# Kernel optimization log

Hardware: AMD Instinct MI355X
Metric: run time of the kernel (lower is better)

## Reference

```python
import jax, jax.numpy as jnp
import numpy as np

B, T, H, OUT = 65536, 24, 64, 2  # batch, window, num_neurons, 2*predicted_step
P_LAYER, P_TIME = 0.2, 0.2


def _mask(k, p):
    # bernoulli(1-p)/(1-p) variational dropout mask on [B, H]
    return jax.random.bernoulli(k, 1.0 - p, (B, H)).astype(jnp.float32) / (1.0 - p)


def setup_inputs() -> dict:
    key = jax.random.key(0)
    ks = jax.random.split(key, 20)
    u = 1.0 / np.sqrt(H)  # torch LSTMCell default init: U(-1/sqrt(H), 1/sqrt(H))
    xav = np.sqrt(2.0 / (B + H))  # xavier_normal_ std for [B, H] states
    inp = {
        "x": jax.random.normal(ks[0], (B, T, 1), dtype=jnp.float32),
        # LSTMCell 1: input dim 1 -> H; gates stacked [i, f, g, o] like torch
        "W_ih1": jax.random.uniform(ks[1], (4 * H, 1), minval=-u, maxval=u),
        "W_hh1": jax.random.uniform(ks[2], (4 * H, H), minval=-u, maxval=u),
        "b_ih1": jax.random.uniform(ks[3], (4 * H,), minval=-u, maxval=u),
        "b_hh1": jax.random.uniform(ks[4], (4 * H,), minval=-u, maxval=u),
        # LSTMCell 2: H -> H
        "W_ih2": jax.random.uniform(ks[5], (4 * H, H), minval=-u, maxval=u),
        "W_hh2": jax.random.uniform(ks[6], (4 * H, H), minval=-u, maxval=u),
        "b_ih2": jax.random.uniform(ks[7], (4 * H,), minval=-u, maxval=u),
        "b_hh2": jax.random.uniform(ks[8], (4 * H,), minval=-u, maxval=u),
        # output Linear H -> 2, bias hard-set to [0.2, -0.2]
        "W_out": jax.random.uniform(ks[9], (OUT, H), minval=-u, maxval=u),
        "b_out": jnp.array([0.2, -0.2], dtype=jnp.float32),
        # xavier_normal_ initialized states
        "h1_0": jax.random.normal(ks[10], (B, H)) * xav,
        "c1_0": jax.random.normal(ks[11], (B, H)) * xav,
        "h2_0": jax.random.normal(ks[12], (B, H)) * xav,
        "c2_0": jax.random.normal(ks[13], (B, H)) * xav,
        # variational dropout masks, fixed across timesteps
        "m_time1": _mask(ks[14], P_TIME),
        "m_time2": _mask(ks[15], P_TIME),
        "m_layer1": _mask(ks[16], P_LAYER),
        "m_layer2": _mask(ks[17], P_LAYER),
    }
    return inp


def _lstm_cell(x, h, c, W_ih, W_hh, b_ih, b_hh):
    gates = x @ W_ih.T + b_ih + h @ W_hh.T + b_hh  # [B, 4H]
    i, f, g, o = jnp.split(gates, 4, axis=-1)
    c_new = jax.nn.sigmoid(f) * c + jax.nn.sigmoid(i) * jnp.tanh(g)
    h_new = jax.nn.sigmoid(o) * jnp.tanh(c_new)
    return h_new, c_new


def reference(x, W_ih1, W_hh1, b_ih1, b_hh1, W_ih2, W_hh2, b_ih2, b_hh2,
              W_out, b_out, h1_0, c1_0, h2_0, c2_0,
              m_time1, m_time2, m_layer1, m_layer2):
    xs = jnp.transpose(x, (1, 0, 2))  # [T, B, 1]

    def step(carry, x_t):
        h1, c1, h2, c2 = carry
        h1, c1 = _lstm_cell(x_t, h1 * m_time1, c1, W_ih1, W_hh1, b_ih1, b_hh1)
        h1 = h1 * m_layer1
        h2, c2 = _lstm_cell(h1, h2 * m_time2, c2, W_ih2, W_hh2, b_ih2, b_hh2)
        h2 = h2 * m_layer2
        return (h1, c1, h2, c2), None

    (h1, c1, h2, c2), _ = jax.lax.scan(step, (h1_0, c1_0, h2_0, c2_0), xs)
    return h2 @ W_out.T + b_out  # [B, 2]
```

## Files before the change

kernel.cpp:

```cpp
#include <hip/hip_runtime.h>


typedef short short8 __attribute__((ext_vector_type(8)));
typedef float f32x4 __attribute__((ext_vector_type(4)));

#define LOG2E 1.44269504088896340736f

__device__ inline float fsig(float x){
  float e = __builtin_amdgcn_exp2f(-LOG2E * x);
  return __builtin_amdgcn_rcpf(1.0f + e);
}
__device__ inline float ftanh(float x){
  float e = __builtin_amdgcn_exp2f((2.0f * LOG2E) * x);
  return 1.0f - 2.0f * __builtin_amdgcn_rcpf(1.0f + e);
}
__device__ inline unsigned short bf16c(float f){
  unsigned uu = __builtin_bit_cast(unsigned, f);
  uu = (uu + 0x7fffu + ((uu >> 16) & 1u)) >> 16;
  return (unsigned short)uu;
}

__global__ __launch_bounds__(256, 2) void vlstm_kernel(
    const float* __restrict__ x,
    const float* __restrict__ Wih1, const float* __restrict__ Whh1,
    const float* __restrict__ bih1, const float* __restrict__ bhh1,
    const float* __restrict__ Wih2, const float* __restrict__ Whh2,
    const float* __restrict__ bih2, const float* __restrict__ bhh2,
    const float* __restrict__ Wout, const float* __restrict__ bout,
    const float* __restrict__ h10, const float* __restrict__ c10,
    const float* __restrict__ h20, const float* __restrict__ c20,
    const float* __restrict__ mt1v, const float* __restrict__ mt2v,
    const float* __restrict__ ml1v, const float* __restrict__ ml2v,
    float* __restrict__ out)
{
  __shared__ unsigned short sh1L[1024];
  __shared__ unsigned short sh1T[1024];
  __shared__ unsigned short sh2T[1024];
  __shared__ float h2f[1024];
  __shared__ float xlds[384];

  const int tid = threadIdx.x;
  const int w  = tid >> 6;
  const int l  = tid & 63;
  const int hi = l >> 4;
  const int lo = l & 15;
  const int u  = 16 * w + lo;

  float b1v[4], b2v[4], wiv[4];
  short8 fr1[4][2], frI[4][2], frH[4][2];
#pragma unroll
  for (int j = 0; j < 4; ++j){
    int n = u + 64 * j;
    b1v[j] = bih1[n] + bhh1[n];
    b2v[j] = bih2[n] + bhh2[n];
    wiv[j] = Wih1[n];
#pragma unroll
    for (int kk = 0; kk < 2; ++kk){
      int off = n * 64 + 32 * kk + 8 * hi;
      short8 s;
#pragma unroll
      for (int e = 0; e < 8; ++e) s[e] = (short)bf16c(Whh1[off + e]);
      fr1[j][kk] = s;
#pragma unroll
      for (int e = 0; e < 8; ++e) s[e] = (short)bf16c(Wih2[off + e]);
      frI[j][kk] = s;
#pragma unroll
      for (int e = 0; e < 8; ++e) s[e] = (short)bf16c(Whh2[off + e]);
      frH[j][kk] = s;
    }
  }

  int wIdx[4];
#pragma unroll
  for (int r = 0; r < 4; ++r){
    int m = 4 * hi + r;
    wIdx[r] = ((m * 128 + u * 2) ^ ((m & 7) << 4)) >> 1;
  }
  int rIdx[2];
#pragma unroll
  for (int kk = 0; kk < 2; ++kk){
    int m = lo;
    rIdx[kk] = ((m * 128 + kk * 64 + hi * 16) ^ ((m & 7) << 4)) >> 1;
  }

  const int wg = blockIdx.x;
#pragma unroll 1
  for (int blk = 0; blk < 8; ++blk){
    const int row0 = wg * 128 + blk * 16;

    for (int idx = tid; idx < 384; idx += 256){
      int r = idx / 24, tt = idx - r * 24;
      xlds[tt * 16 + r] = x[(row0 + r) * 24 + tt];
    }
    float c1r[4], c2r[4], ml1r[4], ml2r[4], mt1r[4], mt2r[4];
#pragma unroll
    for (int r = 0; r < 4; ++r){
      int gofs = (row0 + 4 * hi + r) * 64 + u;
      c1r[r]  = c10[gofs];  c2r[r]  = c20[gofs];
      ml1r[r] = ml1v[gofs]; ml2r[r] = ml2v[gofs];
      mt1r[r] = mt1v[gofs]; mt2r[r] = mt2v[gofs];
      sh1T[wIdx[r]] = bf16c(h10[gofs] * mt1r[r]);
      sh2T[wIdx[r]] = bf16c(h20[gofs] * mt2r[r]);
    }
    __syncthreads();

    short8 a1[2], at2[2];
    a1[0]  = *(const short8*)&sh1T[rIdx[0]];
    a1[1]  = *(const short8*)&sh1T[rIdx[1]];
    at2[0] = *(const short8*)&sh2T[rIdx[0]];
    at2[1] = *(const short8*)&sh2T[rIdx[1]];

#pragma unroll 1
    for (int t = 0; t < 24; ++t){
      float xv[4];
#pragma unroll
      for (int r = 0; r < 4; ++r) xv[r] = xlds[t * 16 + 4 * hi + r];

      f32x4 gt[4];
#pragma unroll
      for (int j = 0; j < 4; ++j){
        f32x4 acc;
#pragma unroll
        for (int r = 0; r < 4; ++r) acc[r] = fmaf(xv[r], wiv[j], b1v[j]);
        acc = __builtin_amdgcn_mfma_f32_16x16x32_bf16(a1[0], fr1[j][0], acc, 0, 0, 0);
        acc = __builtin_amdgcn_mfma_f32_16x16x32_bf16(a1[1], fr1[j][1], acc, 0, 0, 0);
        gt[j] = acc;
      }
#pragma unroll
      for (int r = 0; r < 4; ++r){
        float ti = fsig(gt[0][r]);
        float tf = fsig(gt[1][r]);
        float tg = ftanh(gt[2][r]);
        float to = fsig(gt[3][r]);
        float cn = fmaf(tf, c1r[r], ti * tg);
        c1r[r] = cn;
        float h1l = to * ftanh(cn) * ml1r[r];
        sh1L[wIdx[r]] = bf16c(h1l);
        sh1T[wIdx[r]] = bf16c(h1l * mt1r[r]);
      }
      __syncthreads();

      short8 a2[2];
      a2[0] = *(const short8*)&sh1L[rIdx[0]];
      a2[1] = *(const short8*)&sh1L[rIdx[1]];
      a1[0] = *(const short8*)&sh1T[rIdx[0]];
      a1[1] = *(const short8*)&sh1T[rIdx[1]];

#pragma unroll
      for (int j = 0; j < 4; ++j){
        f32x4 acc;
#pragma unroll
        for (int r = 0; r < 4; ++r) acc[r] = b2v[j];
        acc = __builtin_amdgcn_mfma_f32_16x16x32_bf16(a2[0],  frI[j][0], acc, 0, 0, 0);
        acc = __builtin_amdgcn_mfma_f32_16x16x32_bf16(a2[1],  frI[j][1], acc, 0, 0, 0);
        acc = __builtin_amdgcn_mfma_f32_16x16x32_bf16(at2[0], frH[j][0], acc, 0, 0, 0);
        acc = __builtin_amdgcn_mfma_f32_16x16x32_bf16(at2[1], frH[j][1], acc, 0, 0, 0);
        gt[j] = acc;
      }
#pragma unroll
      for (int r = 0; r < 4; ++r){
        float ti = fsig(gt[0][r]);
        float tf = fsig(gt[1][r]);
        float tg = ftanh(gt[2][r]);
        float to = fsig(gt[3][r]);
        float cn = fmaf(tf, c2r[r], ti * tg);
        c2r[r] = cn;
        float h2l = to * ftanh(cn) * ml2r[r];
        sh2T[wIdx[r]] = bf16c(h2l * mt2r[r]);
        if (t == 23) h2f[(4 * hi + r) * 64 + u] = h2l;
      }
      __syncthreads();

      at2[0] = *(const short8*)&sh2T[rIdx[0]];
      at2[1] = *(const short8*)&sh2T[rIdx[1]];
    }

    if (tid < 32){
      int r = tid & 15, o = tid >> 4;
      float acc = bout[o];
#pragma unroll 8
      for (int uu = 0; uu < 64; ++uu)
        acc = fmaf(h2f[r * 64 + uu], Wout[o * 64 + uu], acc);
      out[(row0 + r) * 2 + o] = acc;
    }
    __syncthreads();
  }
}

extern "C" void kernel_launch(void* const* d_in, const int* in_sizes, int n_in,
                              void* d_out, int out_size, void* d_ws, size_t ws_size,
                              hipStream_t stream)
{
  vlstm_kernel<<<dim3(512), dim3(256), 0, stream>>>(
      (const float*)d_in[0],  (const float*)d_in[1],  (const float*)d_in[2],
      (const float*)d_in[3],  (const float*)d_in[4],  (const float*)d_in[5],
      (const float*)d_in[6],  (const float*)d_in[7],  (const float*)d_in[8],
      (const float*)d_in[9],  (const float*)d_in[10], (const float*)d_in[11],
      (const float*)d_in[12], (const float*)d_in[13], (const float*)d_in[14],
      (const float*)d_in[15], (const float*)d_in[16], (const float*)d_in[17],
      (const float*)d_in[18], (float*)d_out);
}
```

Before: 342.9 us.

## Double-buffer LSTM hidden states to drop a barrier per step, raise occupancy

Hidden-state LDS buffers are double-buffered by timestep parity, so the second __syncthreads per timestep is removed and the layer-2 recurrent input is read after the single barrier. bf16 conversion uses the packed v_cvt_pk_bf16_f32 instruction, and the x loads become one vector load. The grid doubles to 1024 blocks of 4 row-blocks each, and launch bounds ask for 4 blocks per CU, which cuts per-block serial work and may raise occupancy. The risk is register pressure: about 48 weight-fragment VGPRs per thread must now fit a tighter budget and could spill.

```diff
diff --git a/kernel.cpp b/kernel.cpp
--- a/kernel.cpp
+++ b/kernel.cpp
@@ -1,7 +1,7 @@
 #include <hip/hip_runtime.h>
 
 
-typedef short short8 __attribute__((ext_vector_type(8)));
+typedef short short8v __attribute__((ext_vector_type(8)));
 typedef float f32x4 __attribute__((ext_vector_type(4)));
 
 #define LOG2E 1.44269504088896340736f
@@ -20,7 +20,17 @@
   return (unsigned short)uu;
 }
 
-__global__ __launch_bounds__(256, 2) void vlstm_kernel(
+#define PK_STORE4(T, I, f0, f1, f2, f3) do{                       \
+    unsigned _w01, _w23;                                          \
+    asm("v_cvt_pk_bf16_f32 %0, %1, %2" : "=v"(_w01) : "v"(f0), "v"(f1)); \
+    asm("v_cvt_pk_bf16_f32 %0, %1, %2" : "=v"(_w23) : "v"(f2), "v"(f3)); \
+    (T)[(I)[0]] = (unsigned short)_w01;                           \
+    (T)[(I)[1]] = (unsigned short)(_w01 >> 16);                   \
+    (T)[(I)[2]] = (unsigned short)_w23;                           \
+    (T)[(I)[3]] = (unsigned short)(_w23 >> 16);                   \
+  }while(0)
+
+__global__ __launch_bounds__(256, 4) void vlstm_kernel(
     const float* __restrict__ x,
     const float* __restrict__ Wih1, const float* __restrict__ Whh1,
     const float* __restrict__ bih1, const float* __restrict__ bhh1,
@@ -33,9 +43,9 @@
     const float* __restrict__ ml1v, const float* __restrict__ ml2v,
     float* __restrict__ out)
 {
-  __shared__ unsigned short sh1L[1024];
-  __shared__ unsigned short sh1T[1024];
-  __shared__ unsigned short sh2T[1024];
+  __shared__ unsigned short sh1L[2][1024];
+  __shared__ unsigned short sh1T[2][1024];
+  __shared__ unsigned short sh2T[2][1024];
   __shared__ float h2f[1024];
   __shared__ float xlds[384];
 
@@ -47,7 +57,7 @@
   const int u  = 16 * w + lo;
 
   float b1v[4], b2v[4], wiv[4];
-  short8 fr1[4][2], frI[4][2], frH[4][2];
+  short8v fr1[4][2], frI[4][2], frH[4][2];
 #pragma unroll
   for (int j = 0; j < 4; ++j){
     int n = u + 64 * j;
@@ -57,7 +67,7 @@
 #pragma unroll
     for (int kk = 0; kk < 2; ++kk){
       int off = n * 64 + 32 * kk + 8 * hi;
-      short8 s;
+      short8v s;
 #pragma unroll
       for (int e = 0; e < 8; ++e) s[e] = (short)bf16c(Whh1[off + e]);
       fr1[j][kk] = s;
@@ -79,42 +89,41 @@
   int rIdx[2];
 #pragma unroll
   for (int kk = 0; kk < 2; ++kk){
-    int m = lo;
-    rIdx[kk] = ((m * 128 + kk * 64 + hi * 16) ^ ((m & 7) << 4)) >> 1;
-  }
-
-  const int wg = blockIdx.x;
+    rIdx[kk] = ((lo * 128 + kk * 64 + hi * 16) ^ ((lo & 7) << 4)) >> 1;
+  }
+
 #pragma unroll 1
-  for (int blk = 0; blk < 8; ++blk){
-    const int row0 = wg * 128 + blk * 16;
+  for (int blk = 0; blk < 4; ++blk){
+    const int row0 = blockIdx.x * 64 + blk * 16;
 
     for (int idx = tid; idx < 384; idx += 256){
       int r = idx / 24, tt = idx - r * 24;
       xlds[tt * 16 + r] = x[(row0 + r) * 24 + tt];
     }
     float c1r[4], c2r[4], ml1r[4], ml2r[4], mt1r[4], mt2r[4];
+    float h1i[4], h2i[4];
 #pragma unroll
     for (int r = 0; r < 4; ++r){
       int gofs = (row0 + 4 * hi + r) * 64 + u;
       c1r[r]  = c10[gofs];  c2r[r]  = c20[gofs];
       ml1r[r] = ml1v[gofs]; ml2r[r] = ml2v[gofs];
       mt1r[r] = mt1v[gofs]; mt2r[r] = mt2v[gofs];
-      sh1T[wIdx[r]] = bf16c(h10[gofs] * mt1r[r]);
-      sh2T[wIdx[r]] = bf16c(h20[gofs] * mt2r[r]);
-    }
+      h1i[r] = h10[gofs] * mt1r[r];
+      h2i[r] = h20[gofs] * mt2r[r];
+    }
+    PK_STORE4(sh1T[0], wIdx, h1i[0], h1i[1], h1i[2], h1i[3]);
+    PK_STORE4(sh2T[0], wIdx, h2i[0], h2i[1], h2i[2], h2i[3]);
     __syncthreads();
 
-    short8 a1[2], at2[2];
-    a1[0]  = *(const short8*)&sh1T[rIdx[0]];
-    a1[1]  = *(const short8*)&sh1T[rIdx[1]];
-    at2[0] = *(const short8*)&sh2T[rIdx[0]];
-    at2[1] = *(const short8*)&sh2T[rIdx[1]];
-
+    short8v a1[2], at2[2];
+    a1[0] = *(const short8v*)&sh1T[0][rIdx[0]];
+    a1[1] = *(const short8v*)&sh1T[0][rIdx[1]];
+
+    int P = 0;
 #pragma unroll 1
     for (int t = 0; t < 24; ++t){
-      float xv[4];
-#pragma unroll
-      for (int r = 0; r < 4; ++r) xv[r] = xlds[t * 16 + 4 * hi + r];
+      const int Q = P ^ 1;
+      f32x4 xv = *(const f32x4*)&xlds[t * 16 + 4 * hi];
 
       f32x4 gt[4];
 #pragma unroll
@@ -126,6 +135,7 @@
         acc = __builtin_amdgcn_mfma_f32_16x16x32_bf16(a1[1], fr1[j][1], acc, 0, 0, 0);
         gt[j] = acc;
       }
+      float h1l[4], h1t[4];
 #pragma unroll
       for (int r = 0; r < 4; ++r){
         float ti = fsig(gt[0][r]);
@@ -134,17 +144,21 @@
         float to = fsig(gt[3][r]);
         float cn = fmaf(tf, c1r[r], ti * tg);
         c1r[r] = cn;
-        float h1l = to * ftanh(cn) * ml1r[r];
-        sh1L[wIdx[r]] = bf16c(h1l);
-        sh1T[wIdx[r]] = bf16c(h1l * mt1r[r]);
-      }
+        h1l[r] = to * ftanh(cn) * ml1r[r];
+        h1t[r] = h1l[r] * mt1r[r];
+      }
+      PK_STORE4(sh1L[Q], wIdx, h1l[0], h1l[1], h1l[2], h1l[3]);
+      PK_STORE4(sh1T[Q], wIdx, h1t[0], h1t[1], h1t[2], h1t[3]);
+
       __syncthreads();
 
-      short8 a2[2];
-      a2[0] = *(const short8*)&sh1L[rIdx[0]];
-      a2[1] = *(const short8*)&sh1L[rIdx[1]];
-      a1[0] = *(const short8*)&sh1T[rIdx[0]];
-      a1[1] = *(const short8*)&sh1T[rIdx[1]];
+      short8v a2[2];
+      a2[0]  = *(const short8v*)&sh1L[Q][rIdx[0]];
+      a2[1]  = *(const short8v*)&sh1L[Q][rIdx[1]];
+      a1[0]  = *(const short8v*)&sh1T[Q][rIdx[0]];
+      a1[1]  = *(const short8v*)&sh1T[Q][rIdx[1]];
+      at2[0] = *(const short8v*)&sh2T[P][rIdx[0]];
+      at2[1] = *(const short8v*)&sh2T[P][rIdx[1]];
 
 #pragma unroll
       for (int j = 0; j < 4; ++j){
@@ -157,6 +171,7 @@
         acc = __builtin_amdgcn_mfma_f32_16x16x32_bf16(at2[1], frH[j][1], acc, 0, 0, 0);
         gt[j] = acc;
       }
+      float h2t[4];
 #pragma unroll
       for (int r = 0; r < 4; ++r){
         float ti = fsig(gt[0][r]);
@@ -166,14 +181,14 @@
         float cn = fmaf(tf, c2r[r], ti * tg);
         c2r[r] = cn;
         float h2l = to * ftanh(cn) * ml2r[r];
-        sh2T[wIdx[r]] = bf16c(h2l * mt2r[r]);
+        h2t[r] = h2l * mt2r[r];
         if (t == 23) h2f[(4 * hi + r) * 64 + u] = h2l;
       }
-      __syncthreads();
-
-      at2[0] = *(const short8*)&sh2T[rIdx[0]];
-      at2[1] = *(const short8*)&sh2T[rIdx[1]];
-    }
+      PK_STORE4(sh2T[Q], wIdx, h2t[0], h2t[1], h2t[2], h2t[3]);
+
+      P = Q;
+    }
+    __syncthreads();
 
     if (tid < 32){
       int r = tid & 15, o = tid >> 4;
@@ -191,7 +206,7 @@
                               void* d_out, int out_size, void* d_ws, size_t ws_size,
                               hipStream_t stream)
 {
-  vlstm_kernel<<<dim3(512), dim3(256), 0, stream>>>(
+  vlstm_kernel<<<dim3(1024), dim3(256), 0, stream>>>(
       (const float*)d_in[0],  (const float*)d_in[1],  (const float*)d_in[2],
       (const float*)d_in[3],  (const float*)d_in[4],  (const float*)d_in[5],
       (const float*)d_in[6],  (const float*)d_in[7],  (const float*)d_in[8],
```

Result: slower. 1.134 ms (+230.8%).
